# Kernel optimization log

Hardware: AMD Instinct MI355X
Metric: run time of the kernel (lower is better)

The kernel has to match this reference:

```python
import jax, jax.numpy as jnp
import numpy as np

IN_F, OUT_F, GROUP = 4096, 11008, 128
N_GROUPS = IN_F // GROUP  # 32 (in_features divisible by group_size -> no padding)


def setup_inputs() -> dict:
    key = jax.random.key(0)
    kx, kw, ks, kb = jax.random.split(key, 4)
    x = jax.random.normal(kx, (4, 2048, IN_F), dtype=jnp.float32)
    weight_q = jax.random.randint(kw, (OUT_F, IN_F), -128, 128, dtype=jnp.int32).astype(jnp.int8)
    scales = jax.random.uniform(ks, (OUT_F, N_GROUPS), dtype=jnp.float32) * 0.01 + 1e-4
    bias = jax.random.normal(kb, (OUT_F,), dtype=jnp.float32)
    return {"x": x, "weight_q": weight_q, "scales": scales, "bias": bias}


def reference(x, weight_q, scales, bias):
    # Dequantize: group-wise scale along in_features, cast to fp16 (as torch .half())
    W = (weight_q.astype(jnp.float32).reshape(OUT_F, N_GROUPS, GROUP)
         * scales[:, :, None]).reshape(OUT_F, IN_F).astype(jnp.float16)
    # fp16 linear: y = x W^T + b, then back to fp32
    y = jnp.einsum('bsi,oi->bso', x.astype(jnp.float16), W) + bias.astype(jnp.float16)
    return y.astype(jnp.float32)
```

## Files before the change

### kernel.cpp

```cpp
#include <hip/hip_runtime.h>

#define IN_F 4096
#define OUT_F 11008
#define NGROUPS 32
#define M_TOTAL 8192
#define BM 256
#define BN 256
#define BK 64
#define NKT (IN_F / BK)

typedef _Float16 half_t;
typedef unsigned short ushort_t;
typedef __attribute__((ext_vector_type(8))) short short8;
typedef __attribute__((ext_vector_type(4))) float f32x4;
typedef __attribute__((ext_vector_type(4))) int i32x4;
typedef __attribute__((ext_vector_type(4))) unsigned short us4;

typedef __attribute__((address_space(1))) const void gvoid_t;
typedef __attribute__((address_space(3))) void lvoid_t;

__device__ __forceinline__ unsigned short f32_to_bf16_rne(float f) {
  unsigned int u = __builtin_bit_cast(unsigned int, f);
  u += 0x7FFFu + ((u >> 16) & 1u);
  return (unsigned short)(u >> 16);
}

__global__ void convert_x_k(const float* __restrict__ x, ushort_t* __restrict__ xh) {
  const int n4 = M_TOTAL * IN_F / 4;
  int stride = gridDim.x * blockDim.x;
  for (int i = blockIdx.x * blockDim.x + threadIdx.x; i < n4; i += stride) {
    f32x4 v = __builtin_nontemporal_load((const f32x4*)x + i);
    us4 h;
    h[0] = f32_to_bf16_rne(v[0]);
    h[1] = f32_to_bf16_rne(v[1]);
    h[2] = f32_to_bf16_rne(v[2]);
    h[3] = f32_to_bf16_rne(v[3]);
    ((us4*)xh)[i] = h;
  }
}

__global__ void dequant_w_k(const int* __restrict__ wq,
                            const float* __restrict__ scales,
                            ushort_t* __restrict__ wh) {
  int row = blockIdx.x;
  int t = threadIdx.x;
  size_t base = (size_t)row * IN_F + (size_t)t * 8;
  float s = scales[row * NGROUPS + (t >> 4)];
  i32x4 q0 = __builtin_nontemporal_load((const i32x4*)(wq + base));
  i32x4 q1 = __builtin_nontemporal_load((const i32x4*)(wq + base) + 1);
  us4 h0, h1;
#pragma unroll
  for (int j = 0; j < 4; ++j) h0[j] = f32_to_bf16_rne((float)q0[j] * s);
#pragma unroll
  for (int j = 0; j < 4; ++j) h1[j] = f32_to_bf16_rne((float)q1[j] * s);
  *(us4*)(wh + base) = h0;
  *(us4*)(wh + base + 4) = h1;
}


__device__ __forceinline__ void rd4(short8 (&d)[4], const char* base) {
#pragma unroll
  for (int i = 0; i < 4; ++i) d[i] = *(const short8*)(base + i * 1024);
}

__device__ __forceinline__ void mfma16(f32x4 (&acc)[8][4], const short8 (&a)[4],
                                       const short8 (&b)[4], int mh) {
#pragma unroll
  for (int i = 0; i < 4; ++i)
#pragma unroll
    for (int j = 0; j < 4; ++j)
      acc[mh * 4 + i][j] =
          __builtin_amdgcn_mfma_f32_16x16x32_bf16(a[i], b[j], acc[mh * 4 + i][j], 0, 0, 0);
}

#define BAR() __builtin_amdgcn_s_barrier()
#define SB0() __builtin_amdgcn_sched_barrier(0)
#define PRIO1() __builtin_amdgcn_s_setprio(1)
#define PRIO0() __builtin_amdgcn_s_setprio(0)
#define VMCNT(N) asm volatile("s_waitcnt vmcnt(" #N ")" ::: "memory")
#define LGKM(N) asm volatile("s_waitcnt lgkmcnt(" #N ")" ::: "memory")

#define STAGE(OP, KH, KT, S)                                                          \
  do {                                                                                \
    const half_t* g_ = ((OP) ? pBsrc : pAsrc) + (KT) * 64 + (KH) * 32;                \
    char* d_ = (char*)&lds[S][OP][KH][0] + wvoff;                                     \
    __builtin_amdgcn_global_load_lds((gvoid_t*)g_, (lvoid_t*)d_, 16, 0, 0);           \
    __builtin_amdgcn_global_load_lds((gvoid_t*)(g_ + 128 * IN_F),                     \
                                     (lvoid_t*)(d_ + 8192), 16, 0, 0);                \
  } while (0)

#define MPH(SL, KH, S1OP, S1KT, S1SL, S1KH, S2OP, S2KT, S2SL, S2KH, FENCE)   \
  do {                                                                       \
    rd4(a0, (const char*)&lds[SL][0][KH][0] + aoff);                         \
    rd4(a1, (const char*)&lds[SL][0][KH][0] + aoff + 4096);                  \
    rd4(b, (const char*)&lds[SL][1][KH][0] + boff);                          \
    STAGE(S1OP, S1KH, S1KT, S1SL);                                           \
    STAGE(S2OP, S2KH, S2KT, S2SL);                                           \
    LGKM(0); SB0(); PRIO1();                                                 \
    mfma16(acc, a0, b, 0);                                                   \
    mfma16(acc, a1, b, 1);                                                   \
    PRIO0();                                                                 \
    if ((FENCE) == 8) VMCNT(8);                                              \
    BAR(); SB0();                                                            \
  } while (0)

#define MPHN(SL, KH, FENCE)                                                  \
  do {                                                                       \
    rd4(a0, (const char*)&lds[SL][0][KH][0] + aoff);                         \
    rd4(a1, (const char*)&lds[SL][0][KH][0] + aoff + 4096);                  \
    rd4(b, (const char*)&lds[SL][1][KH][0] + boff);                          \
    LGKM(0); SB0(); PRIO1();                                                 \
    mfma16(acc, a0, b, 0);                                                   \
    mfma16(acc, a1, b, 1);                                                   \
    PRIO0();                                                                 \
    if ((FENCE) == 4) VMCNT(4);                                              \
    if ((FENCE) == 0) VMCNT(0);                                              \
    BAR(); SB0();                                                            \
  } while (0)

__global__ __launch_bounds__(512, 1) void gemm_k(const half_t* __restrict__ A,
                                                 const half_t* __restrict__ B,
                                                 const float* __restrict__ bias,
                                                 float* __restrict__ C) {
  __shared__ __align__(16) half_t lds[2][2][2][8192];

  const int tid = threadIdx.x;
  const int lane = tid & 63;
  const int wv = tid >> 6;
  const int wm = wv >> 2;
  const int wn = wv & 3;
  const int wvoff = wv << 10;

  const int nwg = gridDim.x;
  const int perx = nwg >> 3;
  const int L = ((int)blockIdx.x & 7) * perx + ((int)blockIdx.x >> 3);
  const int band = L >> 7;
  const int rr_ = L & 127;
  const int bn0 = band << 2;
  const int cols = (43 - bn0) < 4 ? (43 - bn0) : 4;
  const int bm = rr_ / cols;
  const int bn = bn0 + rr_ % cols;
  const int row0 = bm * BM;
  const int col0 = bn * BN;

  const int c16 = (tid & 3) * 16;
  const int srow = tid >> 2;
  const int clog = c16 ^ ((srow & 6) << 3);
  const int kidx = clog >> 1;
  const half_t* pAsrc = A + (size_t)(row0 + srow) * IN_F + kidx;
  const half_t* pBsrc = B + (size_t)(col0 + srow) * IN_F + kidx;

  const int r16 = lane & 15;
  const int kg = lane >> 4;
  const int arow = wm * 128 + r16;
  const int brow = wn * 64 + r16;
  const int aoff = arow * 64 + ((kg * 16) ^ ((arow & 6) << 3));
  const int boff = brow * 64 + ((kg * 16) ^ ((brow & 6) << 3));

  f32x4 acc[8][4];
#pragma unroll
  for (int m = 0; m < 8; ++m)
#pragma unroll
    for (int n = 0; n < 4; ++n) acc[m][n] = (f32x4){0.f, 0.f, 0.f, 0.f};

  STAGE(0, 0, 0, 0);
  STAGE(1, 0, 0, 0);
  STAGE(0, 1, 0, 0);
  STAGE(1, 1, 0, 0);
  STAGE(0, 0, 1, 1);
  STAGE(1, 0, 1, 1);
  VMCNT(4);
  BAR();
  SB0();

  short8 a0[4], a1[4], b[4];
  for (int u = 0; u < 31; ++u) {
    const int t1 = 2 * u + 1, n0 = 2 * u + 2, n1 = 2 * u + 3;
    MPH(0, 0, 0, t1, 1, 1, 1, t1, 1, 1, 8);
    MPH(0, 1, 0, n0, 0, 0, 1, n0, 0, 0, 8);
    MPH(1, 0, 0, n0, 0, 1, 1, n0, 0, 1, 8);
    MPH(1, 1, 0, n1, 1, 0, 1, n1, 1, 0, 8);
  }
  {
    MPH(0, 0, 0, 63, 1, 1, 1, 63, 1, 1, 8);
    MPHN(0, 1, 4);
    MPHN(1, 0, 0);
    MPHN(1, 1, -1);
  }

  const int kg4 = kg * 4;
#pragma unroll
  for (int nf = 0; nf < 4; ++nf) {
    int col = col0 + wn * 64 + nf * 16 + r16;
    _Float16 bh = (_Float16)bias[col];
#pragma unroll
    for (int mf = 0; mf < 8; ++mf) {
      int rb = row0 + wm * 128 + mf * 16 + kg4;
#pragma unroll
      for (int r = 0; r < 4; ++r) {
        _Float16 v = (_Float16)acc[mf][nf][r] + bh;
        __builtin_nontemporal_store((float)v, &C[(size_t)(rb + r) * OUT_F + col]);
      }
    }
  }
}

__global__ void naive_k(const float* __restrict__ x, const int* __restrict__ wq,
                        const float* __restrict__ scales, const float* __restrict__ bias,
                        float* __restrict__ out) {
  long idx = (long)blockIdx.x * blockDim.x + threadIdx.x;
  if (idx >= (long)M_TOTAL * OUT_F) return;
  int m = (int)(idx / OUT_F);
  int n = (int)(idx % OUT_F);
  float acc = 0.f;
  for (int g = 0; g < NGROUPS; ++g) {
    float s = scales[n * NGROUPS + g];
    for (int k = g * 128; k < (g + 1) * 128; ++k) {
      _Float16 xv = (_Float16)x[(size_t)m * IN_F + k];
      _Float16 wv = (_Float16)((float)wq[(size_t)n * IN_F + k] * s);
      acc += (float)xv * (float)wv;
    }
  }
  _Float16 r = (_Float16)acc + (_Float16)bias[n];
  out[idx] = (float)r;
}

extern "C" void kernel_launch(void* const* d_in, const int* in_sizes, int n_in,
                              void* d_out, int out_size, void* d_ws, size_t ws_size,
                              hipStream_t stream) {
  const float* x = (const float*)d_in[0];
  const int* wq = (const int*)d_in[1];
  const float* scales = (const float*)d_in[2];
  const float* bias = (const float*)d_in[3];
  float* out = (float*)d_out;

  const size_t xh_bytes = (size_t)M_TOTAL * IN_F * 2;
  const size_t wh_bytes = (size_t)OUT_F * IN_F * 2;

  if (ws_size >= xh_bytes + wh_bytes) {
    ushort_t* xh = (ushort_t*)d_ws;
    ushort_t* wh = (ushort_t*)((char*)d_ws + xh_bytes);
    convert_x_k<<<2048, 256, 0, stream>>>(x, xh);
    dequant_w_k<<<OUT_F, 512, 0, stream>>>(wq, scales, wh);
    gemm_k<<<(M_TOTAL / BM) * (OUT_F / BN), 512, 0, stream>>>(
        (const half_t*)xh, (const half_t*)wh, bias, out);
  } else {
    long total = (long)M_TOTAL * OUT_F;
    naive_k<<<(int)((total + 255) / 256), 256, 0, stream>>>(x, wq, scales, bias, out);
  }
}
```

Baseline: 727.5 us.

## Restructure GEMM main loop into 4-stage BK=32 pipeline with register double-buffering

Result: no change. 724.1 us (-0.5%).

```diff
diff --git a/kernel.cpp b/kernel.cpp
--- a/kernel.cpp
+++ b/kernel.cpp
@@ -6,7 +6,7 @@
 #define M_TOTAL 8192
 #define BM 256
 #define BN 256
-#define BK 64
+#define BK 32
 #define NKT (IN_F / BK)
 
 typedef _Float16 half_t;
@@ -58,21 +58,6 @@
 }
 
 
-__device__ __forceinline__ void rd4(short8 (&d)[4], const char* base) {
-#pragma unroll
-  for (int i = 0; i < 4; ++i) d[i] = *(const short8*)(base + i * 1024);
-}
-
-__device__ __forceinline__ void mfma16(f32x4 (&acc)[8][4], const short8 (&a)[4],
-                                       const short8 (&b)[4], int mh) {
-#pragma unroll
-  for (int i = 0; i < 4; ++i)
-#pragma unroll
-    for (int j = 0; j < 4; ++j)
-      acc[mh * 4 + i][j] =
-          __builtin_amdgcn_mfma_f32_16x16x32_bf16(a[i], b[j], acc[mh * 4 + i][j], 0, 0, 0);
-}
-
 #define BAR() __builtin_amdgcn_s_barrier()
 #define SB0() __builtin_amdgcn_sched_barrier(0)
 #define PRIO1() __builtin_amdgcn_s_setprio(1)
@@ -80,56 +65,71 @@
 #define VMCNT(N) asm volatile("s_waitcnt vmcnt(" #N ")" ::: "memory")
 #define LGKM(N) asm volatile("s_waitcnt lgkmcnt(" #N ")" ::: "memory")
 
-#define STAGE(OP, KH, KT, S)                                                          \
-  do {                                                                                \
-    const half_t* g_ = ((OP) ? pBsrc : pAsrc) + (KT) * 64 + (KH) * 32;                \
-    char* d_ = (char*)&lds[S][OP][KH][0] + wvoff;                                     \
-    __builtin_amdgcn_global_load_lds((gvoid_t*)g_, (lvoid_t*)d_, 16, 0, 0);           \
-    __builtin_amdgcn_global_load_lds((gvoid_t*)(g_ + 128 * IN_F),                     \
-                                     (lvoid_t*)(d_ + 8192), 16, 0, 0);                \
-  } while (0)
-
-#define MPH(SL, KH, S1OP, S1KT, S1SL, S1KH, S2OP, S2KT, S2SL, S2KH, FENCE)   \
-  do {                                                                       \
-    rd4(a0, (const char*)&lds[SL][0][KH][0] + aoff);                         \
-    rd4(a1, (const char*)&lds[SL][0][KH][0] + aoff + 4096);                  \
-    rd4(b, (const char*)&lds[SL][1][KH][0] + boff);                          \
-    STAGE(S1OP, S1KH, S1KT, S1SL);                                           \
-    STAGE(S2OP, S2KH, S2KT, S2SL);                                           \
-    LGKM(0); SB0(); PRIO1();                                                 \
-    mfma16(acc, a0, b, 0);                                                   \
-    mfma16(acc, a1, b, 1);                                                   \
-    PRIO0();                                                                 \
-    if ((FENCE) == 8) VMCNT(8);                                              \
-    BAR(); SB0();                                                            \
-  } while (0)
-
-#define MPHN(SL, KH, FENCE)                                                  \
-  do {                                                                       \
-    rd4(a0, (const char*)&lds[SL][0][KH][0] + aoff);                         \
-    rd4(a1, (const char*)&lds[SL][0][KH][0] + aoff + 4096);                  \
-    rd4(b, (const char*)&lds[SL][1][KH][0] + boff);                          \
-    LGKM(0); SB0(); PRIO1();                                                 \
-    mfma16(acc, a0, b, 0);                                                   \
-    mfma16(acc, a1, b, 1);                                                   \
-    PRIO0();                                                                 \
-    if ((FENCE) == 4) VMCNT(4);                                              \
-    if ((FENCE) == 0) VMCNT(0);                                              \
-    BAR(); SB0();                                                            \
+#define GLD(G, D) __builtin_amdgcn_global_load_lds((gvoid_t*)(G), (lvoid_t*)(D), 16, 0, 0)
+
+#define STAGE(KT, S)                                                       \
+  do {                                                                     \
+    const half_t* gA_ = pAsrc + (KT) * 32;                                 \
+    const half_t* gB_ = pBsrc + (KT) * 32;                                 \
+    char* dA_ = (char*)&lds[S][0][0] + t16;                                \
+    char* dB_ = (char*)&lds[S][1][0] + t16;                                \
+    GLD(gA_, dA_);                                                         \
+    GLD(gA_ + 128 * IN_F, dA_ + 8192);                                     \
+    GLD(gB_, dB_);                                                         \
+    GLD(gB_ + 128 * IN_F, dB_ + 8192);                                     \
+  } while (0)
+
+#define RDS(AA, BB, S)                                                     \
+  do {                                                                     \
+    const char* Ab_ = (const char*)&lds[S][0][0];                          \
+    const char* Bb_ = (const char*)&lds[S][1][0];                          \
+    _Pragma("unroll") for (int m_ = 0; m_ < 8; ++m_)                       \
+        AA[m_] = *(const short8*)(Ab_ + aoff + m_ * 1024);                 \
+    _Pragma("unroll") for (int n_ = 0; n_ < 4; ++n_)                       \
+        BB[n_] = *(const short8*)(Bb_ + boff + n_ * 1024);                 \
+  } while (0)
+
+#define MFMA_ALL(AA, BB)                                                   \
+  do {                                                                     \
+    _Pragma("unroll") for (int m_ = 0; m_ < 8; ++m_)                       \
+        _Pragma("unroll") for (int n_ = 0; n_ < 4; ++n_)                   \
+            acc[m_][n_] = __builtin_amdgcn_mfma_f32_16x16x32_bf16(         \
+                AA[m_], BB[n_], acc[m_][n_], 0, 0, 0);                     \
+  } while (0)
+
+#define PH(RA_, RB_, RSLOT, STKT, SSLOT, MA_, MB_, FEN)                    \
+  do {                                                                     \
+    RDS(RA_, RB_, RSLOT);                                                  \
+    STAGE(STKT, SSLOT);                                                    \
+    LGKM(12); SB0(); PRIO1();                                              \
+    MFMA_ALL(MA_, MB_);                                                    \
+    PRIO0();                                                               \
+    if ((FEN) == 4) VMCNT(4);                                              \
+    BAR(); SB0();                                                          \
+  } while (0)
+
+#define PHN(RA_, RB_, RSLOT, MA_, MB_, FEN)                                \
+  do {                                                                     \
+    RDS(RA_, RB_, RSLOT);                                                  \
+    LGKM(12); SB0(); PRIO1();                                              \
+    MFMA_ALL(MA_, MB_);                                                    \
+    PRIO0();                                                               \
+    if ((FEN) == 0) VMCNT(0);                                              \
+    BAR(); SB0();                                                          \
   } while (0)
 
 __global__ __launch_bounds__(512, 1) void gemm_k(const half_t* __restrict__ A,
                                                  const half_t* __restrict__ B,
                                                  const float* __restrict__ bias,
                                                  float* __restrict__ C) {
-  __shared__ __align__(16) half_t lds[2][2][2][8192];
+  __shared__ __align__(16) half_t lds[4][2][8192];
 
   const int tid = threadIdx.x;
   const int lane = tid & 63;
   const int wv = tid >> 6;
   const int wm = wv >> 2;
   const int wn = wv & 3;
-  const int wvoff = wv << 10;
+  const int t16 = tid * 16;
 
   const int nwg = gridDim.x;
   const int perx = nwg >> 3;
@@ -152,10 +152,8 @@
 
   const int r16 = lane & 15;
   const int kg = lane >> 4;
-  const int arow = wm * 128 + r16;
-  const int brow = wn * 64 + r16;
-  const int aoff = arow * 64 + ((kg * 16) ^ ((arow & 6) << 3));
-  const int boff = brow * 64 + ((kg * 16) ^ ((brow & 6) << 3));
+  const int aoff = (wm * 128 + r16) * 64 + ((kg * 16) ^ ((r16 & 6) << 3));
+  const int boff = (wn * 64 + r16) * 64 + ((kg * 16) ^ ((r16 & 6) << 3));
 
   f32x4 acc[8][4];
 #pragma unroll
@@ -163,30 +161,27 @@
 #pragma unroll
     for (int n = 0; n < 4; ++n) acc[m][n] = (f32x4){0.f, 0.f, 0.f, 0.f};
 
-  STAGE(0, 0, 0, 0);
-  STAGE(1, 0, 0, 0);
-  STAGE(0, 1, 0, 0);
-  STAGE(1, 1, 0, 0);
-  STAGE(0, 0, 1, 1);
-  STAGE(1, 0, 1, 1);
+  short8 aA[8], bA[4], aB[8], bB[4];
+
+  STAGE(0, 0);
+  STAGE(1, 1);
+  STAGE(2, 2);
   VMCNT(4);
   BAR();
   SB0();
-
-  short8 a0[4], a1[4], b[4];
-  for (int u = 0; u < 31; ++u) {
-    const int t1 = 2 * u + 1, n0 = 2 * u + 2, n1 = 2 * u + 3;
-    MPH(0, 0, 0, t1, 1, 1, 1, t1, 1, 1, 8);
-    MPH(0, 1, 0, n0, 0, 0, 1, n0, 0, 0, 8);
-    MPH(1, 0, 0, n0, 0, 1, 1, n0, 0, 1, 8);
-    MPH(1, 1, 0, n1, 1, 0, 1, n1, 1, 0, 8);
-  }
-  {
-    MPH(0, 0, 0, 63, 1, 1, 1, 63, 1, 1, 8);
-    MPHN(0, 1, 4);
-    MPHN(1, 0, 0);
-    MPHN(1, 1, -1);
-  }
+  RDS(aA, bA, 0);
+
+  for (int u = 0; u < 62; ++u) {
+    const int t0 = 2 * u;
+    PH(aB, bB, (t0 + 1) & 3, t0 + 3, (t0 + 3) & 3, aA, bA, 4);
+    PH(aA, bA, (t0 + 2) & 3, t0 + 4, (t0 + 4) & 3, aB, bB, 4);
+  }
+  PH(aB, bB, 1, 127, 3, aA, bA, 4);
+  PHN(aA, bA, 2, aB, bB, 0);
+  PHN(aB, bB, 3, aA, bA, -1);
+  LGKM(0);
+  SB0();
+  MFMA_ALL(aB, bB);
 
   const int kg4 = kg * 4;
 #pragma unroll
```
